# Optimization experiments

Measured on AMD Instinct MI355X. Metric: run time of the kernel, lower is better.

Reference implementation:

```python
import jax, jax.numpy as jnp
import numpy as np

B, S, D = 2, 2048, 4096
NH, NKV = 32, 8
HD = D // NH          # 128
NREP = NH // NKV      # 4
SCALE = HD ** -0.5


def setup_inputs() -> dict:
    key = jax.random.key(0)
    kx, kq, kk, kv, ko = jax.random.split(key, 5)
    s = 0.02
    return {
        "x": jax.random.normal(kx, (B, S, D), dtype=jnp.float32),
        "wq": jax.random.normal(kq, (D, NH * HD), dtype=jnp.float32) * s,
        "wk": jax.random.normal(kk, (D, NKV * HD), dtype=jnp.float32) * s,
        "wv": jax.random.normal(kv, (D, NKV * HD), dtype=jnp.float32) * s,
        "wo": jax.random.normal(ko, (NH * HD, D), dtype=jnp.float32) * s,
    }


def reference(x, wq, wk, wv, wo):
    b, s, _ = x.shape
    q = (x @ wq).reshape(b, s, NH, HD)    # b s h d
    k = (x @ wk).reshape(b, s, NKV, HD)   # b s kv d
    v = (x @ wv).reshape(b, s, NKV, HD)
    # GQA: repeat kv heads to match query heads
    k = jnp.repeat(k, NREP, axis=2)       # b s h d
    v = jnp.repeat(v, NREP, axis=2)
    scores = jnp.einsum("bihd,bjhd->bhij", q, k) * SCALE  # b h i j
    causal = jnp.tril(jnp.ones((s, s), dtype=bool))
    scores = jnp.where(causal, scores, jnp.finfo(scores.dtype).min)
    attn = jax.nn.softmax(scores, axis=-1)
    out = jnp.einsum("bhij,bjhd->bihd", attn, v)          # b s h d
    out = out.reshape(b, s, NH * HD)
    return out @ wo
```

## Files before the change

kernel.cpp:

```cpp
#include <hip/hip_runtime.h>
#include <cstdint>
#include <cstddef>

typedef __bf16 bf16x8 __attribute__((ext_vector_type(8)));
typedef float  f32x4  __attribute__((ext_vector_type(4)));
typedef unsigned short u16;

#define SCALE_F 0.08838834764831845f
#define QSCALE_F (0.08838834764831845f * 1.4426950408889634f)

__device__ __forceinline__ u16 f2bf(float f) {
  unsigned int u = __builtin_bit_cast(unsigned int, f);
  u += 0x7fffu + ((u >> 16) & 1u);
  return (u16)(u >> 16);
}

__device__ __forceinline__ unsigned cvt_pk_bf16(float lo, float hi) {
  unsigned r;
  asm("v_cvt_pk_bf16_f32 %0, %1, %2" : "=v"(r) : "v"(lo), "v"(hi));
  return r;
}

__device__ __forceinline__ void load_lds16(const void* g, void* l) {
  __builtin_amdgcn_global_load_lds((const __attribute__((address_space(1))) void*)g,
                                   (__attribute__((address_space(3))) void*)l,
                                   16, 0, 0);
}

__global__ __launch_bounds__(256) void prep_all(const float* __restrict__ x,
                                                const float* __restrict__ wq,
                                                const float* __restrict__ wk,
                                                const float* __restrict__ wv,
                                                const float* __restrict__ wo,
                                                u16* __restrict__ xb,
                                                u16* __restrict__ wqkvT,
                                                u16* __restrict__ woT) {
  __shared__ float tile[32][33];
  const int tid = threadIdx.x;
  int blk = blockIdx.x;
  if (blk < 2048) {
    int idx = blk * 256 + tid;
    const int n4 = 4096 * 4096 / 4;
    for (; idx < n4; idx += 2048 * 256) {
      float4 v = ((const float4*)x)[idx];
      uint2 pk;
      pk.x = (unsigned)f2bf(v.x) | ((unsigned)f2bf(v.y) << 16);
      pk.y = (unsigned)f2bf(v.z) | ((unsigned)f2bf(v.w) << 16);
      ((uint2*)xb)[idx] = pk;
    }
    return;
  }
  blk -= 2048;
  const float* in; u16* out; long C; int nbx; float scale;
  if (blk < 16384)      { in = wq; out = wqkvT;                          C = 4096; nbx = 128; scale = QSCALE_F; }
  else if (blk < 20480) { blk -= 16384; in = wk; out = wqkvT + (size_t)4096 * 4096; C = 1024; nbx = 32; scale = 1.f; }
  else if (blk < 24576) { blk -= 20480; in = wv; out = wqkvT + (size_t)5120 * 4096; C = 1024; nbx = 32; scale = 1.f; }
  else                  { blk -= 24576; in = wo; out = woT;              C = 4096; nbx = 128; scale = 1.f; }
  const long R = 4096;
  const int tx = tid & 31, ty = tid >> 5;
  const long c0 = (long)(blk % nbx) * 32, r0 = (long)(blk / nbx) * 32;
#pragma unroll
  for (int i = 0; i < 4; i++)
    tile[ty + i * 8][tx] = in[(r0 + ty + i * 8) * C + c0 + tx];
  __syncthreads();
#pragma unroll
  for (int i = 0; i < 4; i++)
    out[(c0 + ty + i * 8) * R + r0 + tx] = f2bf(tile[tx][ty + i * 8] * scale);
}

__global__ __launch_bounds__(256) void transpose_u16(const u16* __restrict__ in,
                                                     u16* __restrict__ out,
                                                     int R, int C, int ldi, int ldo) {
  __shared__ u16 tile[32][33];
  const int tx = threadIdx.x, ty = threadIdx.y;
  const long c0 = (long)blockIdx.x * 32, r0 = (long)blockIdx.y * 32;
#pragma unroll
  for (int i = 0; i < 4; i++)
    tile[ty + i * 8][tx] = in[(r0 + ty + i * 8) * (long)ldi + c0 + tx];
  __syncthreads();
#pragma unroll
  for (int i = 0; i < 4; i++)
    out[(c0 + ty + i * 8) * (long)ldo + r0 + tx] = tile[tx][ty + i * 8];
}

#define STGA(db, ks, KC) { int kc_ = (KC) < K ? (KC) : 0; \
    load_lds16(gA0 + kc_, &SA[db][ks][s0 * 8]); \
    load_lds16(gA1 + kc_, &SA[db][ks][s1 * 8]); }
#define STGB(db, ks, KC) { int kc_ = (KC) < K ? (KC) : 0; \
    load_lds16(gB0 + kc_, &SB[db][ks][s0 * 8]); \
    load_lds16(gB1 + kc_, &SB[db][ks][s1 * 8]); }

#define PH(MBc, AU, BU, DBn, KSn, MBn, AN, RDB, BN_, STG, DOVM) { \
    STG; \
    if (DOVM) asm volatile("s_waitcnt vmcnt(8)"); \
    __builtin_amdgcn_s_barrier(); \
    _Pragma("unroll") for (int mm = 0; mm < 4; mm++) \
      AN[mm] = *(const bf16x8*)(&SA[DBn][KSn][aoff + (MBn + mm) * 512]); \
    if (RDB) { \
      _Pragma("unroll") for (int n = 0; n < 4; n++) \
        BN_[n] = *(const bf16x8*)(&SB[DBn][KSn][boff + n * 512]); \
    } \
    __builtin_amdgcn_s_setprio(1); \
    _Pragma("unroll") for (int mm = 0; mm < 4; mm++) \
      _Pragma("unroll") for (int n = 0; n < 4; n++) \
        acc[MBc + mm][n] = __builtin_amdgcn_mfma_f32_16x16x32_bf16(AU[mm], BU[n], acc[MBc + mm][n], 0, 0, 0); \
    __builtin_amdgcn_s_setprio(0); \
  }

template <int BF16_OUT>
__device__ __forceinline__ void gemm_body(const u16* __restrict__ A,
                                          const u16* __restrict__ Bt,
                                          void* __restrict__ Cv,
                                          int M, int N, int K, int NBX) {
  __shared__ u16 SA[2][2][8192];
  __shared__ u16 SB[2][2][8192];
  const int tid = threadIdx.x;
  const int lane = tid & 63;
  const int g = lane >> 4, r16 = lane & 15;
  const int wid = tid >> 6;
  const int wm = wid >> 2, wn = wid & 3;

  const int cpx = gridDim.x >> 3;
  const int lin = (blockIdx.x & 7) * cpx + (blockIdx.x >> 3);
  const long bm = (long)(lin / NBX) * 256;
  const long bn = (long)(lin % NBX) * 256;

  const int s0 = tid, s1 = 512 + tid;
  const int rp0 = s0 >> 3, ci0 = (s0 & 7) ^ (rp0 & 7);
  const int rp1 = s1 >> 3, ci1 = (s1 & 7) ^ (rp1 & 7);
  const long gr0 = rp0 * 2 + (ci0 >> 2), gc0 = (ci0 & 3) * 8;
  const long gr1 = rp1 * 2 + (ci1 >> 2), gc1 = (ci1 & 3) * 8;
  const u16* gA0 = A + (bm + gr0) * K + gc0;
  const u16* gA1 = A + (bm + gr1) * K + gc1;
  const u16* gB0 = Bt + (bn + gr0) * K + gc0;
  const u16* gB1 = Bt + (bn + gr1) * K + gc1;

  const int rA = wm * 128 + r16;
  const int aoff = (rA >> 1) * 64 + ((((rA & 1) << 2) + g) ^ ((rA >> 1) & 7)) * 8;
  const int rB = wn * 64 + r16;
  const int boff = (rB >> 1) * 64 + ((((rB & 1) << 2) + g) ^ ((rB >> 1) & 7)) * 8;

  f32x4 acc[8][4];
#pragma unroll
  for (int m = 0; m < 8; m++)
#pragma unroll
    for (int n = 0; n < 4; n++)
#pragma unroll
      for (int j = 0; j < 4; j++) acc[m][n][j] = 0.f;

  bf16x8 afrX[4], afrY[4], bfrX[4], bfrY[4];

  STGA(0, 0, 0); STGB(0, 0, 0);
  STGA(0, 1, 32); STGB(0, 1, 32);
  STGA(1, 0, 64); STGB(1, 0, 64);
  __builtin_amdgcn_sched_barrier(0);
  asm volatile("s_waitcnt vmcnt(0)" ::: "memory");
  __builtin_amdgcn_s_barrier();

#pragma unroll
  for (int mm = 0; mm < 4; mm++)
    afrX[mm] = *(const bf16x8*)(&SA[0][0][aoff + mm * 512]);
#pragma unroll
  for (int n = 0; n < 4; n++)
    bfrX[n] = *(const bf16x8*)(&SB[0][0][boff + n * 512]);

  for (int it = 0; it < K / 128; it++) {
    const int t0 = it * 128;
    PH(0, afrX, bfrX, 0, 0, 4, afrY, 0, bfrY, STGA(1, 1, t0 + 96), 0);
    PH(4, afrY, bfrX, 0, 1, 0, afrX, 1, bfrY, STGB(1, 1, t0 + 96), 1);
    PH(0, afrX, bfrY, 0, 1, 4, afrY, 0, bfrX, STGA(0, 0, t0 + 128), 0);
    PH(4, afrY, bfrY, 1, 0, 0, afrX, 1, bfrX, STGB(0, 0, t0 + 128), 1);
    PH(0, afrX, bfrX, 1, 0, 4, afrY, 0, bfrY, STGA(0, 1, t0 + 160), 0);
    PH(4, afrY, bfrX, 1, 1, 0, afrX, 1, bfrY, STGB(0, 1, t0 + 160), 1);
    PH(0, afrX, bfrY, 1, 1, 4, afrY, 0, bfrX, STGA(1, 0, t0 + 192), 0);
    PH(4, afrY, bfrY, 0, 0, 0, afrX, 1, bfrX, STGB(1, 0, t0 + 192), 1);
  }

  const long crow = bm + wm * 128 + g * 4;
  const long ccol = bn + wn * 64 + r16;
  if (BF16_OUT) {
    u16* C = (u16*)Cv;
#pragma unroll
    for (int m = 0; m < 8; m++)
#pragma unroll
      for (int n = 0; n < 4; n++)
#pragma unroll
        for (int j = 0; j < 4; j++)
          C[(crow + m * 16 + j) * (long)N + ccol + n * 16] = f2bf(acc[m][n][j]);
  } else {
    float* C = (float*)Cv;
#pragma unroll
    for (int m = 0; m < 8; m++)
#pragma unroll
      for (int n = 0; n < 4; n++)
#pragma unroll
        for (int j = 0; j < 4; j++)
          C[(crow + m * 16 + j) * (long)N + ccol + n * 16] = acc[m][n][j];
  }
}

__global__ __launch_bounds__(512, 2) void gemm_qkv(const u16* __restrict__ A,
                                                   const u16* __restrict__ Bt,
                                                   void* __restrict__ Cv,
                                                   int M, int N, int K, int NBX) {
  gemm_body<1>(A, Bt, Cv, M, N, K, NBX);
}
__global__ __launch_bounds__(512, 2) void gemm_wo(const u16* __restrict__ A,
                                                  const u16* __restrict__ Bt,
                                                  void* __restrict__ Cv,
                                                  int M, int N, int K, int NBX) {
  gemm_body<0>(A, Bt, Cv, M, N, K, NBX);
}

__global__ __launch_bounds__(512, 2) void attn_fwd(const u16* __restrict__ QK,
                                                   const u16* __restrict__ VT,
                                                   u16* __restrict__ Og) {
  __shared__ u16 Ks[2][64 * 128];
  __shared__ u16 Vs[2][128 * 64];
  __shared__ u16 Ps[8][2][16 * 64];
  const int tid = threadIdx.x;
  const int lane = tid & 63;
  const int w = tid >> 6;
  const int g = lane >> 4, r16 = lane & 15;
  const int qtA = blockIdx.x;
  const int qtB = 15 - qtA;
  const int h2 = blockIdx.y, b = blockIdx.z;
  const int h0 = h2 * 2;
  const int kvh = h0 >> 2;

  const u16* kcol   = QK + (long)b * 2048 * 6144 + 4096 + kvh * 128;
  const u16* vb_ptr = VT + (long)kvh * 128 * 4096 + (long)b * 2048;

  const int nktA = 2 * (qtA + 1);
  const int ntot = 34;

  int qbase = qtA * 128;
  int qlo = qbase + w * 16;
  int qrow = qlo + r16;

  bf16x8 qf[2][4];
  auto load_q = [&]() {
    const u16* qp = QK + ((long)(b * 2048 + qrow)) * 6144 + h0 * 128 + g * 8;
#pragma unroll
    for (int hh = 0; hh < 2; hh++)
#pragma unroll
      for (int kc = 0; kc < 4; kc++)
        qf[hh][kc] = *(const bf16x8*)(qp + hh * 128 + kc * 32);
  };
  load_q();

  f32x4 oacc[2][8];
  float mrun[2], lrun[2];
  auto reinit = [&]() {
#pragma unroll
    for (int hh = 0; hh < 2; hh++) {
#pragma unroll
      for (int dt = 0; dt < 8; dt++)
#pragma unroll
        for (int j = 0; j < 4; j++) oacc[hh][dt][j] = 0.f;
      mrun[hh] = -__builtin_inff();
      lrun[hh] = 0.f;
    }
  };
  reinit();

  auto finalize = [&]() {
#pragma unroll
    for (int hh = 0; hh < 2; hh++) {
      float li[4];
#pragma unroll
      for (int j = 0; j < 4; j++)
        li[j] = 1.f / __shfl(lrun[hh], (lane & 48) + g * 4 + j);
      u16* op = Og + ((long)(b * 2048 + qbase + w * 16 + g * 4)) * 4096 + (h0 + hh) * 128 + r16;
#pragma unroll
      for (int dt = 0; dt < 8; dt++)
#pragma unroll
        for (int j = 0; j < 4; j++)
          op[(long)j * 4096 + dt * 16] = f2bf(oacc[hh][dt][j] * li[j]);
    }
  };

  auto stage = [&](int bf, int kb) {
#pragma unroll
    for (int i = 0; i < 2; i++) {
      int slot = i * 512 + tid;
      int r = slot >> 4, cs = slot & 15;
      int ck = (cs & 8) | ((cs ^ r) & 7);
      load_lds16(kcol + (long)(kb + r) * 6144 + ck * 8, &Ks[bf][slot * 8]);
      int d = slot >> 3, c8 = slot & 7;
      int cv = (c8 ^ d) & 7;
      load_lds16(vb_ptr + (long)d * 4096 + kb + cv * 8, &Vs[bf][slot * 8]);
    }
  };

  stage(0, 0);
  __syncthreads();
  int cur = 0;

  for (int i = 0; i < ntot; i++) {
    if (i == nktA) {
      finalize();
      qbase = qtB * 128;
      qlo = qbase + w * 16;
      qrow = qlo + r16;
      load_q();
      reinit();
    }
    const int kt = (i < nktA) ? i : i - nktA;
    const int kb = kt * 64;
    if (i + 1 < ntot) {
      const int ktn = (i + 1 < nktA) ? i + 1 : i + 1 - nktA;
      stage(cur ^ 1, ktn * 64);
    }

    if (kb <= qlo + 15) {
      const bool masked = (kb + 63 > qlo);

#pragma unroll
      for (int hh = 0; hh < 2; hh++) {
        f32x4 st[4];
#pragma unroll
        for (int t = 0; t < 4; t++)
#pragma unroll
          for (int j = 0; j < 4; j++) st[t][j] = 0.f;
#pragma unroll
        for (int t = 0; t < 4; t++) {
          const int r = t * 16 + r16;
#pragma unroll
          for (int kc = 0; kc < 4; kc++) {
            int c = kc * 4 + g;
            int cz = (c & 8) | ((c ^ r) & 7);
            bf16x8 kf = *(const bf16x8*)(&Ks[cur][r * 128 + cz * 8]);
            st[t] = __builtin_amdgcn_mfma_f32_16x16x32_bf16(kf, qf[hh][kc], st[t], 0, 0, 0);
          }
        }

        float p[4][4];
        float tmax = -__builtin_inff();
#pragma unroll
        for (int t = 0; t < 4; t++)
#pragma unroll
          for (int j = 0; j < 4; j++) {
            float s = st[t][j];
            if (masked) {
              int kv = kb + t * 16 + g * 4 + j;
              s = (kv > qrow) ? -__builtin_inff() : s;
            }
            p[t][j] = s;
            tmax = fmaxf(tmax, s);
          }
        tmax = fmaxf(tmax, __shfl_xor(tmax, 16));
        tmax = fmaxf(tmax, __shfl_xor(tmax, 32));

        if (!__all(tmax <= mrun[hh] + 8.f)) {
          const float mnew = fmaxf(mrun[hh], tmax);
          const float esc = exp2f(mrun[hh] - mnew);
          float es[4];
#pragma unroll
          for (int j = 0; j < 4; j++) es[j] = __shfl(esc, (lane & 48) + g * 4 + j);
#pragma unroll
          for (int dt = 0; dt < 8; dt++)
#pragma unroll
            for (int j = 0; j < 4; j++) oacc[hh][dt][j] *= es[j];
          lrun[hh] *= esc;
          mrun[hh] = mnew;
        }
        float psum = 0.f;
#pragma unroll
        for (int t = 0; t < 4; t++)
#pragma unroll
          for (int j = 0; j < 4; j++) {
            float e = exp2f(p[t][j] - mrun[hh]);
            p[t][j] = e;
            psum += e;
          }
        psum += __shfl_xor(psum, 16);
        psum += __shfl_xor(psum, 32);
        lrun[hh] += psum;

        u16* pw = Ps[w][hh];
#pragma unroll
        for (int t = 0; t < 4; t++)
#pragma unroll
          for (int pp = 0; pp < 2; pp++) {
            int kvl = t * 16 + g * 4 + pp * 2;
            unsigned val = cvt_pk_bf16(p[t][pp * 2], p[t][pp * 2 + 1]);
            int off = r16 * 128 + ((kvl * 2) ^ ((r16 & 7) << 4));
            *(unsigned int*)((char*)pw + off) = val;
          }

#pragma unroll
        for (int kc2 = 0; kc2 < 2; kc2++) {
          int c = kc2 * 4 + g;
          int cp = c ^ (r16 & 7);
          bf16x8 pa = *(const bf16x8*)(pw + r16 * 64 + cp * 8);
#pragma unroll
          for (int dt = 0; dt < 8; dt++) {
            int d = dt * 16 + r16;
            int cz = c ^ (d & 7);
            bf16x8 vf = *(const bf16x8*)(&Vs[cur][d * 64 + cz * 8]);
            oacc[hh][dt] = __builtin_amdgcn_mfma_f32_16x16x32_bf16(pa, vf, oacc[hh][dt], 0, 0, 0);
          }
        }
      }
    }

    __syncthreads();
    cur ^= 1;
  }

  finalize();
}

extern "C" void kernel_launch(void* const* d_in, const int* in_sizes, int n_in,
                              void* d_out, int out_size, void* d_ws, size_t ws_size,
                              hipStream_t stream) {
  (void)in_sizes; (void)n_in; (void)out_size; (void)ws_size;
  const float* x  = (const float*)d_in[0];
  const float* wq = (const float*)d_in[1];
  const float* wk = (const float*)d_in[2];
  const float* wv = (const float*)d_in[3];
  const float* wo = (const float*)d_in[4];
  float* out = (float*)d_out;

  u16* xb     = (u16*)d_ws;
  u16* wqkvT  = xb    + (size_t)4096 * 4096;
  u16* woT    = wqkvT + (size_t)6144 * 4096;
  u16* qkv    = woT   + (size_t)4096 * 4096;
  u16* vT     = qkv   + (size_t)4096 * 6144;
  u16* attn   = xb;

  prep_all<<<43008, 256, 0, stream>>>(x, wq, wk, wv, wo, xb, wqkvT, woT);

  gemm_qkv<<<384, 512, 0, stream>>>(xb, wqkvT, qkv, 4096, 6144, 4096, 24);
  transpose_u16<<<dim3(32, 128), dim3(32, 8), 0, stream>>>(qkv + 5120, vT, 4096, 1024, 6144, 4096);

  attn_fwd<<<dim3(8, 16, 2), 512, 0, stream>>>(qkv, vT, attn);

  gemm_wo<<<256, 512, 0, stream>>>(attn, woT, out, 4096, 4096, 4096, 16);
}
```

Measured before the change: 525.5 us.

## Split QKV projection into separate Q GEMM and simple KV GEMM kernel

Breaks the fused QKV GEMM (384 blocks over N=6144) into a Q GEMM on the existing tuned kernel (256 blocks) and a new simple 128x128 single-buffered MFMA GEMM for K/V. Buffers are relaid out so attention reads separate Q and KV arrays. The weight-prep transpose now handles 64x32 tiles with packed 32-bit bf16 stores, halving the block count. The goal is to even out the grid tail across CUs and cut prep store traffic, but the new KV GEMM is unpipelined and likely far slower per FLOP than the tuned kernel.

```diff
diff --git a/kernel.cpp b/kernel.cpp
--- a/kernel.cpp
+++ b/kernel.cpp
@@ -33,9 +33,10 @@
                                                 const float* __restrict__ wv,
                                                 const float* __restrict__ wo,
                                                 u16* __restrict__ xb,
-                                                u16* __restrict__ wqkvT,
+                                                u16* __restrict__ wqT,
+                                                u16* __restrict__ wkvT,
                                                 u16* __restrict__ woT) {
-  __shared__ float tile[32][33];
+  __shared__ float tile[64][33];
   const int tid = threadIdx.x;
   int blk = blockIdx.x;
   if (blk < 2048) {
@@ -52,20 +53,29 @@
   }
   blk -= 2048;
   const float* in; u16* out; long C; int nbx; float scale;
-  if (blk < 16384)      { in = wq; out = wqkvT;                          C = 4096; nbx = 128; scale = QSCALE_F; }
-  else if (blk < 20480) { blk -= 16384; in = wk; out = wqkvT + (size_t)4096 * 4096; C = 1024; nbx = 32; scale = 1.f; }
-  else if (blk < 24576) { blk -= 20480; in = wv; out = wqkvT + (size_t)5120 * 4096; C = 1024; nbx = 32; scale = 1.f; }
-  else                  { blk -= 24576; in = wo; out = woT;              C = 4096; nbx = 128; scale = 1.f; }
+  if (blk < 8192)       { in = wq; out = wqT;                           C = 4096; nbx = 128; scale = QSCALE_F; }
+  else if (blk < 10240) { blk -= 8192;  in = wk; out = wkvT;                          C = 1024; nbx = 32; scale = 1.f; }
+  else if (blk < 12288) { blk -= 10240; in = wv; out = wkvT + (size_t)1024 * 4096;    C = 1024; nbx = 32; scale = 1.f; }
+  else                  { blk -= 12288; in = wo; out = woT;                           C = 4096; nbx = 128; scale = 1.f; }
   const long R = 4096;
-  const int tx = tid & 31, ty = tid >> 5;
-  const long c0 = (long)(blk % nbx) * 32, r0 = (long)(blk / nbx) * 32;
-#pragma unroll
-  for (int i = 0; i < 4; i++)
-    tile[ty + i * 8][tx] = in[(r0 + ty + i * 8) * C + c0 + tx];
+  const long c0 = (long)(blk % nbx) * 32, r0 = (long)(blk / nbx) * 64;
+  {
+    const int tx = tid & 31, ty = tid >> 5;
+#pragma unroll
+    for (int i = 0; i < 8; i++)
+      tile[ty + i * 8][tx] = in[(r0 + ty + i * 8) * C + c0 + tx];
+  }
   __syncthreads();
-#pragma unroll
-  for (int i = 0; i < 4; i++)
-    out[(c0 + ty + i * 8) * R + r0 + tx] = f2bf(tile[tx][ty + i * 8] * scale);
+  {
+    const int tx = tid & 31, cy = tid >> 5;
+#pragma unroll
+    for (int i = 0; i < 4; i++) {
+      int col = cy + i * 8;
+      unsigned val = (unsigned)f2bf(tile[2 * tx][col] * scale) |
+                     ((unsigned)f2bf(tile[2 * tx + 1][col] * scale) << 16);
+      *(unsigned*)&out[(c0 + col) * R + r0 + 2 * tx] = val;
+    }
+  }
 }
 
 __global__ __launch_bounds__(256) void transpose_u16(const u16* __restrict__ in,
@@ -81,6 +91,77 @@
 #pragma unroll
   for (int i = 0; i < 4; i++)
     out[(c0 + ty + i * 8) * (long)ldo + r0 + tx] = tile[tx][ty + i * 8];
+}
+
+template <int BF16_OUT>
+__global__ __launch_bounds__(256) void gemm_bt(const u16* __restrict__ A,
+                                               const u16* __restrict__ Bt,
+                                               void* __restrict__ Cv,
+                                               int M, int N, int K) {
+  __shared__ u16 As[128 * 32];
+  __shared__ u16 Bs[128 * 32];
+  const int tid = threadIdx.x;
+  const int lane = tid & 63;
+  const int g = lane >> 4, r16 = lane & 15;
+  const int wid = tid >> 6;
+  const int wr = wid >> 1, wc = wid & 1;
+  const long bm = (long)blockIdx.y * 128, bn = (long)blockIdx.x * 128;
+
+  const u16* gA = A + (bm + (tid >> 2)) * (long)K + (tid & 3) * 8;
+  const u16* gB = Bt + (bn + (tid >> 2)) * (long)K + (tid & 3) * 8;
+  u16* lA = As + tid * 8;
+  u16* lB = Bs + tid * 8;
+
+  f32x4 acc[4][4];
+#pragma unroll
+  for (int m = 0; m < 4; m++)
+#pragma unroll
+    for (int n = 0; n < 4; n++)
+#pragma unroll
+      for (int j = 0; j < 4; j++) acc[m][n][j] = 0.f;
+
+  for (int k0 = 0; k0 < K; k0 += 32) {
+    load_lds16(gA + k0, lA);
+    load_lds16(gA + 64 * (long)K + k0, lA + 256 * 8);
+    load_lds16(gB + k0, lB);
+    load_lds16(gB + 64 * (long)K + k0, lB + 256 * 8);
+    __syncthreads();
+    bf16x8 af[4], bfr[4];
+#pragma unroll
+    for (int m = 0; m < 4; m++)
+      af[m] = *(const bf16x8*)(As + (wr * 64 + m * 16 + r16) * 32 + g * 8);
+#pragma unroll
+    for (int n = 0; n < 4; n++)
+      bfr[n] = *(const bf16x8*)(Bs + (wc * 64 + n * 16 + r16) * 32 + g * 8);
+#pragma unroll
+    for (int m = 0; m < 4; m++)
+#pragma unroll
+      for (int n = 0; n < 4; n++)
+        acc[m][n] = __builtin_amdgcn_mfma_f32_16x16x32_bf16(af[m], bfr[n], acc[m][n], 0, 0, 0);
+    __syncthreads();
+  }
+
+  const long crow = bm + wr * 64 + g * 4;
+  const long ccol = bn + wc * 64 + r16;
+  if (BF16_OUT) {
+    u16* C = (u16*)Cv;
+#pragma unroll
+    for (int m = 0; m < 4; m++)
+#pragma unroll
+      for (int n = 0; n < 4; n++)
+#pragma unroll
+        for (int j = 0; j < 4; j++)
+          C[(crow + m * 16 + j) * (long)N + ccol + n * 16] = f2bf(acc[m][n][j]);
+  } else {
+    float* C = (float*)Cv;
+#pragma unroll
+    for (int m = 0; m < 4; m++)
+#pragma unroll
+      for (int n = 0; n < 4; n++)
+#pragma unroll
+        for (int j = 0; j < 4; j++)
+          C[(crow + m * 16 + j) * (long)N + ccol + n * 16] = acc[m][n][j];
+  }
 }
 
 #define STGA(db, ks, KC) { int kc_ = (KC) < K ? (KC) : 0; \
@@ -199,10 +280,10 @@
   }
 }
 
-__global__ __launch_bounds__(512, 2) void gemm_qkv(const u16* __restrict__ A,
-                                                   const u16* __restrict__ Bt,
-                                                   void* __restrict__ Cv,
-                                                   int M, int N, int K, int NBX) {
+__global__ __launch_bounds__(512, 2) void gemm_q(const u16* __restrict__ A,
+                                                 const u16* __restrict__ Bt,
+                                                 void* __restrict__ Cv,
+                                                 int M, int N, int K, int NBX) {
   gemm_body<1>(A, Bt, Cv, M, N, K, NBX);
 }
 __global__ __launch_bounds__(512, 2) void gemm_wo(const u16* __restrict__ A,
@@ -212,7 +293,8 @@
   gemm_body<0>(A, Bt, Cv, M, N, K, NBX);
 }
 
-__global__ __launch_bounds__(512, 2) void attn_fwd(const u16* __restrict__ QK,
+__global__ __launch_bounds__(512, 2) void attn_fwd(const u16* __restrict__ Q,
+                                                   const u16* __restrict__ KV,
                                                    const u16* __restrict__ VT,
                                                    u16* __restrict__ Og) {
   __shared__ u16 Ks[2][64 * 128];
@@ -228,7 +310,7 @@
   const int h0 = h2 * 2;
   const int kvh = h0 >> 2;
 
-  const u16* kcol   = QK + (long)b * 2048 * 6144 + 4096 + kvh * 128;
+  const u16* kcol   = KV + (long)b * 2048 * 2048 + kvh * 128;
   const u16* vb_ptr = VT + (long)kvh * 128 * 4096 + (long)b * 2048;
 
   const int nktA = 2 * (qtA + 1);
@@ -240,7 +322,7 @@
 
   bf16x8 qf[2][4];
   auto load_q = [&]() {
-    const u16* qp = QK + ((long)(b * 2048 + qrow)) * 6144 + h0 * 128 + g * 8;
+    const u16* qp = Q + ((long)(b * 2048 + qrow)) * 4096 + h0 * 128 + g * 8;
 #pragma unroll
     for (int hh = 0; hh < 2; hh++)
 #pragma unroll
@@ -286,7 +368,7 @@
       int slot = i * 512 + tid;
       int r = slot >> 4, cs = slot & 15;
       int ck = (cs & 8) | ((cs ^ r) & 7);
-      load_lds16(kcol + (long)(kb + r) * 6144 + ck * 8, &Ks[bf][slot * 8]);
+      load_lds16(kcol + (long)(kb + r) * 2048 + ck * 8, &Ks[bf][slot * 8]);
       int d = slot >> 3, c8 = slot & 7;
       int cv = (c8 ^ d) & 7;
       load_lds16(vb_ptr + (long)d * 4096 + kb + cv * 8, &Vs[bf][slot * 8]);
@@ -423,19 +505,22 @@
   const float* wo = (const float*)d_in[4];
   float* out = (float*)d_out;
 
-  u16* xb     = (u16*)d_ws;
-  u16* wqkvT  = xb    + (size_t)4096 * 4096;
-  u16* woT    = wqkvT + (size_t)6144 * 4096;
-  u16* qkv    = woT   + (size_t)4096 * 4096;
-  u16* vT     = qkv   + (size_t)4096 * 6144;
-  u16* attn   = xb;
-
-  prep_all<<<43008, 256, 0, stream>>>(x, wq, wk, wv, wo, xb, wqkvT, woT);
-
-  gemm_qkv<<<384, 512, 0, stream>>>(xb, wqkvT, qkv, 4096, 6144, 4096, 24);
-  transpose_u16<<<dim3(32, 128), dim3(32, 8), 0, stream>>>(qkv + 5120, vT, 4096, 1024, 6144, 4096);
-
-  attn_fwd<<<dim3(8, 16, 2), 512, 0, stream>>>(qkv, vT, attn);
+  u16* xb    = (u16*)d_ws;
+  u16* wqT   = xb   + (size_t)4096 * 4096;
+  u16* wkvT  = wqT  + (size_t)4096 * 4096;
+  u16* woT   = wkvT + (size_t)2048 * 4096;
+  u16* qb    = woT  + (size_t)4096 * 4096;
+  u16* kvb   = qb   + (size_t)4096 * 4096;
+  u16* vT    = kvb  + (size_t)4096 * 2048;
+  u16* attn  = xb;
+
+  prep_all<<<22528, 256, 0, stream>>>(x, wq, wk, wv, wo, xb, wqT, wkvT, woT);
+
+  gemm_q<<<256, 512, 0, stream>>>(xb, wqT, qb, 4096, 4096, 4096, 16);
+  gemm_bt<1><<<dim3(16, 32), 256, 0, stream>>>(xb, wkvT, kvb, 4096, 2048, 4096);
+  transpose_u16<<<dim3(32, 128), dim3(32, 8), 0, stream>>>(kvb + 1024, vT, 4096, 1024, 2048, 4096);
+
+  attn_fwd<<<dim3(8, 16, 2), 512, 0, stream>>>(qb, kvb, vT, attn);
 
   gemm_wo<<<256, 512, 0, stream>>>(attn, woT, out, 4096, 4096, 4096, 16);
 }
```

Result: no change. 529.6 us (+0.8%).
